# Optimization experiments

Hardware: AMD Instinct MI355X
Metric: run time of the kernel (lower is better)

Reference implementation:

```python
import jax, jax.numpy as jnp
import numpy as np

B, L, S = 8192, 1024, 3
OUTSIDE, TM_HELIX, INSIDE = 0, 1, 2


def setup_inputs() -> dict:
    key = jax.random.key(0)
    k1, k2 = jax.random.split(key)
    emissions = jax.random.normal(k1, (B, L, S), dtype=jnp.float32)
    tags = jax.random.randint(k2, (B, L), 0, S)
    mask = jnp.ones((B, L), dtype=jnp.float32)
    t = np.zeros((S, S), dtype=np.float32)
    t[OUTSIDE, INSIDE] = -5.0
    t[INSIDE, OUTSIDE] = -5.0
    t[OUTSIDE, TM_HELIX] = 1.0
    t[INSIDE, TM_HELIX] = 1.0
    t[TM_HELIX, OUTSIDE] = 1.0
    t[TM_HELIX, INSIDE] = 1.0
    transitions = jnp.asarray(t)
    return {"emissions": emissions, "mask": mask, "transitions": transitions, "tags": tags}


def _score_sentence(emissions, tags, mask, transitions):
    # emission score of the gold tag at every position: (B, L)
    em_score = jnp.take_along_axis(emissions, tags[..., None], axis=2)[..., 0]
    # transition score between consecutive gold tags: (B, L-1)
    trans_score = transitions[tags[:, :-1], tags[:, 1:]]
    return em_score[:, 0] * mask[:, 0] + jnp.sum(
        (trans_score + em_score[:, 1:]) * mask[:, 1:], axis=1
    )


def _forward_alg(emissions, mask, transitions):
    def step(alpha, xs):
        em_t, m_t = xs  # (B, S), (B,)
        # scores[b, i, j] = alpha[b, i] + T[i, j] + em_t[b, j]
        scores = alpha[:, :, None] + transitions[None, :, :] + em_t[:, None, :]
        new_alpha = jax.nn.logsumexp(scores, axis=1)
        alpha = jnp.where(m_t[:, None] > 0, new_alpha, alpha)
        return alpha, None

    alpha0 = emissions[:, 0, :]
    xs = (jnp.swapaxes(emissions[:, 1:, :], 0, 1),  # (L-1, B, S)
          jnp.swapaxes(mask[:, 1:], 0, 1))          # (L-1, B)
    alpha, _ = jax.lax.scan(step, alpha0, xs)
    return jax.nn.logsumexp(alpha, axis=1)  # (B,)


def reference(emissions, mask, transitions, tags):
    logZ = _forward_alg(emissions, mask, transitions)
    gold = _score_sentence(emissions, tags, mask, transitions)
    return jnp.mean(logZ - gold)
```

## Files before the change

### kernel.cpp

```cpp
#include <hip/hip_runtime.h>


#define LOG2E 1.4426950408889634f
#define LN2   0.6931471805599453f

constexpr int B = 8192;
constexpr int L = 1024;
constexpr int SEQS_PER_BLOCK = 4;

__device__ __forceinline__ float fexp2(float x) { return __builtin_amdgcn_exp2f(x); }
__device__ __forceinline__ float flog2(float x) { return __builtin_amdgcn_logf(x); }

__device__ __forceinline__ float mux3(float x0, float x1, float x2, int i) {
  return (i == 0) ? x0 : ((i == 1) ? x1 : x2);
}
__device__ __forceinline__ float trmux(const float* __restrict__ T2, int p, int c) {
  const float r0 = mux3(T2[0], T2[1], T2[2], c);
  const float r1 = mux3(T2[3], T2[4], T2[5], c);
  const float r2 = mux3(T2[6], T2[7], T2[8], c);
  return mux3(r0, r1, r2, p);
}

__device__ __forceinline__ void matmul3(float* __restrict__ D,
                                        const float* __restrict__ A,
                                        const float* __restrict__ Bm) {
  #pragma unroll
  for (int i = 0; i < 3; ++i)
    #pragma unroll
    for (int j = 0; j < 3; ++j)
      D[i * 3 + j] = A[i * 3 + 0] * Bm[0 * 3 + j] +
                     A[i * 3 + 1] * Bm[1 * 3 + j] +
                     A[i * 3 + 2] * Bm[2 * 3 + j];
}

__device__ __forceinline__ void renorm3(float* __restrict__ P, float& scale) {
  float m = P[0];
  #pragma unroll
  for (int e = 1; e < 9; ++e) m = fmaxf(m, P[e]);
  int ex;
  (void)frexpf(m, &ex);
  #pragma unroll
  for (int e = 0; e < 9; ++e) P[e] = ldexpf(P[e], -ex);
  scale += (float)ex;
}

__global__ __launch_bounds__(256, 4) void crf_main(
    const float* __restrict__ em, const float* __restrict__ mask,
    const float* __restrict__ trans, const int* __restrict__ tags,
    float* __restrict__ out) {
  const int lane = threadIdx.x & 63;
  const int wid = threadIdx.x >> 6;
  const int b = blockIdx.x * SEQS_PER_BLOCK + wid;

  float T2[9], tk[9];
  #pragma unroll
  for (int e = 0; e < 9; ++e) {
    T2[e] = trans[e] * LOG2E;
    tk[e] = fexp2(T2[e]);
  }

  const float4* em4 = (const float4*)(em + (size_t)b * (L * 3));
  const float4* mk4 = (const float4*)(mask + (size_t)b * L);
  const int4*   tg4 = (const int4*)(tags + (size_t)b * L);

  float P[9] = {1.f, 0.f, 0.f, 0.f, 1.f, 0.f, 0.f, 0.f, 1.f};
  float scale = 0.f, gold = 0.f;
  float a0 = 0.f, a1 = 0.f, a2 = 0.f;
  float e0_sel = 0.f, mk0 = 0.f;
  int tag0 = 0, prev = 0;

  #pragma unroll
  for (int g = 0; g < 4; ++g) {
    const float4 x0 = em4[lane * 12 + 3 * g + 0];
    const float4 x1 = em4[lane * 12 + 3 * g + 1];
    const float4 x2 = em4[lane * 12 + 3 * g + 2];
    const float4 mm = mk4[lane * 4 + g];
    const int4   tt = tg4[lane * 4 + g];
    const float ef[12] = {x0.x, x0.y, x0.z, x0.w, x1.x, x1.y, x1.z, x1.w,
                          x2.x, x2.y, x2.z, x2.w};
    const float mf[4] = {mm.x, mm.y, mm.z, mm.w};
    const int   tf[4] = {tt.x, tt.y, tt.z, tt.w};

    #pragma unroll
    for (int j = 0; j < 4; ++j) {
      const int s = 4 * g + j;
      const float ev0 = ef[3 * j + 0] * LOG2E;
      const float ev1 = ef[3 * j + 1] * LOG2E;
      const float ev2 = ef[3 * j + 2] * LOG2E;
      const float m = mf[j];
      const int cur = tf[j];

      const float e = mux3(ev0, ev1, ev2, cur);
      if (s == 0) {
        e0_sel = e; mk0 = m; tag0 = cur;
      } else {
        gold = fmaf(trmux(T2, prev, cur) + e, m, gold);
      }
      prev = cur;

      const float w0 = fexp2(ev0);
      const float w1 = fexp2(ev1);
      const float w2 = fexp2(ev2);
      if (s == 0) { a0 = w0; a1 = w1; a2 = w2; }
      const bool act = (m > 0.f) && !(s == 0 && lane == 0);
      const float M[9] = {tk[0] * w0, tk[1] * w1, tk[2] * w2,
                          tk[3] * w0, tk[4] * w1, tk[5] * w2,
                          tk[6] * w0, tk[7] * w1, tk[8] * w2};
      float N[9];
      matmul3(N, P, M);
      #pragma unroll
      for (int e2 = 0; e2 < 9; ++e2) P[e2] = act ? N[e2] : P[e2];

      if (s == 7 || s == 15) renorm3(P, scale);
    }
  }

  const int prevLast = __shfl_up(prev, 1);
  if (lane == 0) gold = fmaf(e0_sel, mk0, gold);
  else           gold = fmaf(trmux(T2, prevLast, tag0) + e0_sel, mk0, gold);
  #pragma unroll
  for (int d = 1; d < 64; d <<= 1) gold += __shfl_xor(gold, d, 64);

  #pragma unroll
  for (int d = 1; d < 64; d <<= 1) {
    float o[9];
    #pragma unroll
    for (int e = 0; e < 9; ++e) o[e] = __shfl_xor(P[e], d, 64);
    const float osc = __shfl_xor(scale, d, 64);
    const bool later = (lane & d) != 0;
    float A[9], Bm[9];
    #pragma unroll
    for (int e = 0; e < 9; ++e) {
      A[e]  = later ? o[e] : P[e];
      Bm[e] = later ? P[e] : o[e];
    }
    float N[9];
    matmul3(N, A, Bm);
    #pragma unroll
    for (int e = 0; e < 9; ++e) P[e] = N[e];
    scale += osc;
  }

  __shared__ float red[SEQS_PER_BLOCK];
  if (lane == 0) {
    const float z = a0 * (P[0] + P[1] + P[2]) +
                    a1 * (P[3] + P[4] + P[5]) +
                    a2 * (P[6] + P[7] + P[8]);
    red[wid] = LN2 * (scale + flog2(z) - gold);
  }
  __syncthreads();
  if (threadIdx.x == 0) {
    const float s = red[0] + red[1] + red[2] + red[3];
    atomicAdd(out, s * (1.0f / (float)B));
  }
}

extern "C" void kernel_launch(void* const* d_in, const int* in_sizes, int n_in,
                              void* d_out, int out_size, void* d_ws, size_t ws_size,
                              hipStream_t stream) {
  const float* em    = (const float*)d_in[0];
  const float* mask  = (const float*)d_in[1];
  const float* trans = (const float*)d_in[2];
  const int*   tags  = (const int*)d_in[3];
  float* out = (float*)d_out;

  hipMemsetAsync(out, 0, sizeof(float), stream);
  crf_main<<<B / SEQS_PER_BLOCK, 256, 0, stream>>>(em, mask, trans, tags, out);
}
```

Before: 197.2 us.

## Split sequences into chunks per lane with LDS staging and separate combine kernel

Replaces the one-wave-per-sequence scheme, which used a 64-lane shuffle scan of 3x3 matrices, with one lane per sequence handling a 128-position chunk. There are 8 chunks per sequence, and the chunk results go to a workspace. Emission, mask and tag loads are staged through LDS with a one-step register prefetch to keep global accesses coalesced. A second kernel composes the chunk matrices sequentially per sequence and reduces. The mask select becomes arithmetic blending inside the matrix step. In exchange the change adds a workspace round trip and a second launch, and only 512 blocks of 128 threads run in the main kernel, which may underfill the GPU.

```diff
diff --git a/kernel.cpp b/kernel.cpp
--- a/kernel.cpp
+++ b/kernel.cpp
@@ -5,154 +5,205 @@
 #define LN2   0.6931471805599453f
 
 constexpr int B = 8192;
-constexpr int L = 1024;
-constexpr int SEQS_PER_BLOCK = 4;
-
-__device__ __forceinline__ float fexp2(float x) { return __builtin_amdgcn_exp2f(x); }
-__device__ __forceinline__ float flog2(float x) { return __builtin_amdgcn_logf(x); }
-
-__device__ __forceinline__ float mux3(float x0, float x1, float x2, int i) {
-  return (i == 0) ? x0 : ((i == 1) ? x1 : x2);
-}
-__device__ __forceinline__ float trmux(const float* __restrict__ T2, int p, int c) {
-  const float r0 = mux3(T2[0], T2[1], T2[2], c);
-  const float r1 = mux3(T2[3], T2[4], T2[5], c);
-  const float r2 = mux3(T2[6], T2[7], T2[8], c);
-  return mux3(r0, r1, r2, p);
-}
-
-__device__ __forceinline__ void matmul3(float* __restrict__ D,
-                                        const float* __restrict__ A,
-                                        const float* __restrict__ Bm) {
-  #pragma unroll
-  for (int i = 0; i < 3; ++i)
-    #pragma unroll
-    for (int j = 0; j < 3; ++j)
-      D[i * 3 + j] = A[i * 3 + 0] * Bm[0 * 3 + j] +
-                     A[i * 3 + 1] * Bm[1 * 3 + j] +
-                     A[i * 3 + 2] * Bm[2 * 3 + j];
-}
-
-__device__ __forceinline__ void renorm3(float* __restrict__ P, float& scale) {
+constexpr int NCHUNK = 8;
+constexpr int NSUB = 32;
+constexpr int EM_ST = 14;
+constexpr int MK_ST = 6;
+constexpr int TG_ST = 6;
+constexpr int NF = 13;
+
+__device__ __forceinline__ float fexp2(float x){ return __builtin_amdgcn_exp2f(x); }
+__device__ __forceinline__ float flog2(float x){ return __builtin_amdgcn_logf(x); }
+__device__ __forceinline__ float mux3(float a,float b,float c,int i){
+  return i==0 ? a : (i==1 ? b : c);
+}
+__device__ __forceinline__ float trmux(const float* __restrict__ T2,int p,int c){
+  const float r0 = mux3(T2[0],T2[1],T2[2],c);
+  const float r1 = mux3(T2[3],T2[4],T2[5],c);
+  const float r2 = mux3(T2[6],T2[7],T2[8],c);
+  return mux3(r0,r1,r2,p);
+}
+
+__device__ __forceinline__ void stepP(float* __restrict__ P,
+                                      const float* __restrict__ tk,
+                                      float w0, float w1, float w2, float g){
+  const float c1 = 1.f - g;
+  const float u0 = w0*g, u1 = w1*g, u2 = w2*g;
+  float N0,N1,N2,N3,N4,N5,N6,N7,N8;
+  { const float m0=fmaf(tk[0],u0,c1), m1=tk[3]*u0, m2=tk[6]*u0;
+    N0 = P[0]*m0 + P[1]*m1 + P[2]*m2;
+    N3 = P[3]*m0 + P[4]*m1 + P[5]*m2;
+    N6 = P[6]*m0 + P[7]*m1 + P[8]*m2; }
+  { const float m0=tk[1]*u1, m1=fmaf(tk[4],u1,c1), m2=tk[7]*u1;
+    N1 = P[0]*m0 + P[1]*m1 + P[2]*m2;
+    N4 = P[3]*m0 + P[4]*m1 + P[5]*m2;
+    N7 = P[6]*m0 + P[7]*m1 + P[8]*m2; }
+  { const float m0=tk[2]*u2, m1=tk[5]*u2, m2=fmaf(tk[8],u2,c1);
+    N2 = P[0]*m0 + P[1]*m1 + P[2]*m2;
+    N5 = P[3]*m0 + P[4]*m1 + P[5]*m2;
+    N8 = P[6]*m0 + P[7]*m1 + P[8]*m2; }
+  P[0]=N0; P[1]=N1; P[2]=N2; P[3]=N3; P[4]=N4;
+  P[5]=N5; P[6]=N6; P[7]=N7; P[8]=N8;
+}
+
+__device__ __forceinline__ void renorm3(float* __restrict__ P, float& scale){
   float m = P[0];
   #pragma unroll
-  for (int e = 1; e < 9; ++e) m = fmaxf(m, P[e]);
+  for (int e=1;e<9;++e) m = fmaxf(m, P[e]);
   int ex;
   (void)frexpf(m, &ex);
   #pragma unroll
-  for (int e = 0; e < 9; ++e) P[e] = ldexpf(P[e], -ex);
+  for (int e=0;e<9;++e) P[e] = ldexpf(P[e], -ex);
   scale += (float)ex;
 }
 
-__global__ __launch_bounds__(256, 4) void crf_main(
+__global__ __launch_bounds__(128) void crf_chunk(
     const float* __restrict__ em, const float* __restrict__ mask,
     const float* __restrict__ trans, const int* __restrict__ tags,
+    float* __restrict__ ws) {
+  __shared__ float s_em[2][64*EM_ST];
+  __shared__ float s_mk[2][64*MK_ST];
+  __shared__ int   s_tg[2][64*TG_ST];
+
+  const int lane = threadIdx.x & 63;
+  const int wid  = threadIdx.x >> 6;
+  const int sg   = blockIdx.x & 63;
+  const int c    = blockIdx.x >> 6;
+  const int seqbase = sg*128 + wid*64;
+  const int seq = seqbase + lane;
+  const bool c0 = (c == 0);
+
+  float* emL = s_em[wid];
+  float* mkL = s_mk[wid];
+  int*   tgL = s_tg[wid];
+
+  float T2[9], tk[9];
+  #pragma unroll
+  for (int e=0;e<9;++e){ T2[e] = trans[e]*LOG2E; tk[e] = fexp2(T2[e]); }
+
+  const float4* em4 = (const float4*)em;
+  const float4* mk4 = (const float4*)mask;
+  const int4*   tg4 = (const int4*)tags;
+
+  int wa0, wa1, wa2; size_t gb0, gb1, gb2;
+  {
+    int K, r, col;
+    K = lane;        r = K/3; col = K-3*r; wa0 = r*EM_ST+col*4; gb0 = (size_t)(seqbase+r)*768 + (size_t)c*96 + col;
+    K = 64 + lane;   r = K/3; col = K-3*r; wa1 = r*EM_ST+col*4; gb1 = (size_t)(seqbase+r)*768 + (size_t)c*96 + col;
+    K = 128 + lane;  r = K/3; col = K-3*r; wa2 = r*EM_ST+col*4; gb2 = (size_t)(seqbase+r)*768 + (size_t)c*96 + col;
+  }
+  const size_t mb = (size_t)seq*256 + (size_t)c*32;
+
+  float4 sA = em4[gb0], sBv = em4[gb1], sC = em4[gb2];
+  float4 sM = mk4[mb];
+  int4   sT = tg4[mb];
+
+  float P[9] = {1.f,0.f,0.f, 0.f,1.f,0.f, 0.f,0.f,1.f};
+  float scale = 0.f, gold = 0.f;
+  float a0 = 0.f, a1 = 0.f, a2 = 0.f, m0s = 0.f;
+  int tag0 = 0, prev = 0;
+
+  for (int sub = 0; sub < NSUB; ++sub) {
+    { float2* w = (float2*)&emL[wa0]; w[0]=make_float2(sA.x,sA.y);  w[1]=make_float2(sA.z,sA.w); }
+    { float2* w = (float2*)&emL[wa1]; w[0]=make_float2(sBv.x,sBv.y);w[1]=make_float2(sBv.z,sBv.w); }
+    { float2* w = (float2*)&emL[wa2]; w[0]=make_float2(sC.x,sC.y);  w[1]=make_float2(sC.z,sC.w); }
+    { float2* w = (float2*)&mkL[lane*MK_ST]; w[0]=make_float2(sM.x,sM.y); w[1]=make_float2(sM.z,sM.w); }
+    { int2*   w = (int2*)&tgL[lane*TG_ST];   w[0]=make_int2(sT.x,sT.y);   w[1]=make_int2(sT.z,sT.w); }
+
+    if (sub + 1 < NSUB) {
+      const int o = (sub+1)*3;
+      sA = em4[gb0 + o]; sBv = em4[gb1 + o]; sC = em4[gb2 + o];
+      sM = mk4[mb + sub + 1];
+      sT = tg4[mb + sub + 1];
+    }
+
+    const float2* ep = (const float2*)&emL[lane*EM_ST];
+    const float2* mp = (const float2*)&mkL[lane*MK_ST];
+    const int2*   tp = (const int2*)&tgL[lane*TG_ST];
+    #pragma unroll
+    for (int p = 0; p < 2; ++p) {
+      const float2 ea = ep[3*p], eb = ep[3*p+1], ec = ep[3*p+2];
+      const float2 mm = mp[p];
+      const int2   tt = tp[p];
+      #pragma unroll
+      for (int jj = 0; jj < 2; ++jj) {
+        const float ev0 = (jj ? eb.y : ea.x) * LOG2E;
+        const float ev1 = (jj ? ec.x : ea.y) * LOG2E;
+        const float ev2 = (jj ? ec.y : eb.x) * LOG2E;
+        const float m   = jj ? mm.y : mm.x;
+        const int   cur = jj ? tt.y : tt.x;
+        const bool first = (sub == 0) && (p == 0) && (jj == 0);
+
+        const float e = mux3(ev0, ev1, ev2, cur);
+        if (first) { tag0 = cur; m0s = m; gold = e * m; }
+        else       gold = fmaf(trmux(T2, prev, cur) + e, m, gold);
+        prev = cur;
+
+        const float w0 = fexp2(ev0), w1 = fexp2(ev1), w2 = fexp2(ev2);
+        if (first && c0) { a0 = w0; a1 = w1; a2 = w2; }
+        const bool act = (m > 0.f) && !(first && c0);
+        stepP(P, tk, w0, w1, w2, act ? 1.f : 0.f);
+      }
+    }
+    if (sub & 1) renorm3(P, scale);
+  }
+
+  float* f = ws + (size_t)c*NF*8192 + seq;
+  f[0*8192]=P[0]; f[1*8192]=P[1]; f[2*8192]=P[2];
+  f[3*8192]=P[3]; f[4*8192]=P[4]; f[5*8192]=P[5];
+  f[6*8192]=P[6]; f[7*8192]=P[7]; f[8*8192]=P[8];
+  f[9*8192]=scale; f[10*8192]=gold; f[11*8192]=m0s;
+  f[12*8192]=(float)(tag0 + 4*prev);
+  if (c0) {
+    float* aw = ws + (size_t)NF*NCHUNK*8192;
+    aw[seq] = a0; aw[8192+seq] = a1; aw[2*8192+seq] = a2;
+  }
+}
+
+__global__ __launch_bounds__(256) void crf_combine(
+    const float* __restrict__ trans, const float* __restrict__ ws,
     float* __restrict__ out) {
-  const int lane = threadIdx.x & 63;
-  const int wid = threadIdx.x >> 6;
-  const int b = blockIdx.x * SEQS_PER_BLOCK + wid;
-
-  float T2[9], tk[9];
-  #pragma unroll
-  for (int e = 0; e < 9; ++e) {
-    T2[e] = trans[e] * LOG2E;
-    tk[e] = fexp2(T2[e]);
-  }
-
-  const float4* em4 = (const float4*)(em + (size_t)b * (L * 3));
-  const float4* mk4 = (const float4*)(mask + (size_t)b * L);
-  const int4*   tg4 = (const int4*)(tags + (size_t)b * L);
-
-  float P[9] = {1.f, 0.f, 0.f, 0.f, 1.f, 0.f, 0.f, 0.f, 1.f};
-  float scale = 0.f, gold = 0.f;
-  float a0 = 0.f, a1 = 0.f, a2 = 0.f;
-  float e0_sel = 0.f, mk0 = 0.f;
-  int tag0 = 0, prev = 0;
-
-  #pragma unroll
-  for (int g = 0; g < 4; ++g) {
-    const float4 x0 = em4[lane * 12 + 3 * g + 0];
-    const float4 x1 = em4[lane * 12 + 3 * g + 1];
-    const float4 x2 = em4[lane * 12 + 3 * g + 2];
-    const float4 mm = mk4[lane * 4 + g];
-    const int4   tt = tg4[lane * 4 + g];
-    const float ef[12] = {x0.x, x0.y, x0.z, x0.w, x1.x, x1.y, x1.z, x1.w,
-                          x2.x, x2.y, x2.z, x2.w};
-    const float mf[4] = {mm.x, mm.y, mm.z, mm.w};
-    const int   tf[4] = {tt.x, tt.y, tt.z, tt.w};
-
-    #pragma unroll
-    for (int j = 0; j < 4; ++j) {
-      const int s = 4 * g + j;
-      const float ev0 = ef[3 * j + 0] * LOG2E;
-      const float ev1 = ef[3 * j + 1] * LOG2E;
-      const float ev2 = ef[3 * j + 2] * LOG2E;
-      const float m = mf[j];
-      const int cur = tf[j];
-
-      const float e = mux3(ev0, ev1, ev2, cur);
-      if (s == 0) {
-        e0_sel = e; mk0 = m; tag0 = cur;
-      } else {
-        gold = fmaf(trmux(T2, prev, cur) + e, m, gold);
-      }
-      prev = cur;
-
-      const float w0 = fexp2(ev0);
-      const float w1 = fexp2(ev1);
-      const float w2 = fexp2(ev2);
-      if (s == 0) { a0 = w0; a1 = w1; a2 = w2; }
-      const bool act = (m > 0.f) && !(s == 0 && lane == 0);
-      const float M[9] = {tk[0] * w0, tk[1] * w1, tk[2] * w2,
-                          tk[3] * w0, tk[4] * w1, tk[5] * w2,
-                          tk[6] * w0, tk[7] * w1, tk[8] * w2};
-      float N[9];
-      matmul3(N, P, M);
-      #pragma unroll
-      for (int e2 = 0; e2 < 9; ++e2) P[e2] = act ? N[e2] : P[e2];
-
-      if (s == 7 || s == 15) renorm3(P, scale);
-    }
-  }
-
-  const int prevLast = __shfl_up(prev, 1);
-  if (lane == 0) gold = fmaf(e0_sel, mk0, gold);
-  else           gold = fmaf(trmux(T2, prevLast, tag0) + e0_sel, mk0, gold);
-  #pragma unroll
-  for (int d = 1; d < 64; d <<= 1) gold += __shfl_xor(gold, d, 64);
-
-  #pragma unroll
-  for (int d = 1; d < 64; d <<= 1) {
-    float o[9];
-    #pragma unroll
-    for (int e = 0; e < 9; ++e) o[e] = __shfl_xor(P[e], d, 64);
-    const float osc = __shfl_xor(scale, d, 64);
-    const bool later = (lane & d) != 0;
-    float A[9], Bm[9];
-    #pragma unroll
-    for (int e = 0; e < 9; ++e) {
-      A[e]  = later ? o[e] : P[e];
-      Bm[e] = later ? P[e] : o[e];
-    }
-    float N[9];
-    matmul3(N, A, Bm);
-    #pragma unroll
-    for (int e = 0; e < 9; ++e) P[e] = N[e];
-    scale += osc;
-  }
-
-  __shared__ float red[SEQS_PER_BLOCK];
-  if (lane == 0) {
-    const float z = a0 * (P[0] + P[1] + P[2]) +
-                    a1 * (P[3] + P[4] + P[5]) +
-                    a2 * (P[6] + P[7] + P[8]);
-    red[wid] = LN2 * (scale + flog2(z) - gold);
-  }
+  __shared__ float red[4];
+  const int seq = blockIdx.x*256 + threadIdx.x;
+
+  float T2[9];
+  #pragma unroll
+  for (int e=0;e<9;++e) T2[e] = trans[e]*LOG2E;
+
+  const float* aw = ws + (size_t)NF*NCHUNK*8192;
+  float al0 = aw[seq], al1 = aw[8192+seq], al2 = aw[2*8192+seq];
+  float sc = 0.f, gold = 0.f;
+  int lastTag = 0;
+
+  for (int c = 0; c < NCHUNK; ++c) {
+    const float* f = ws + (size_t)c*NF*8192 + seq;
+    const float p0=f[0*8192], p1=f[1*8192], p2=f[2*8192];
+    const float p3=f[3*8192], p4=f[4*8192], p5=f[5*8192];
+    const float p6=f[6*8192], p7=f[7*8192], p8=f[8*8192];
+    const float csc=f[9*8192], gp=f[10*8192], m0=f[11*8192];
+    const int tp = (int)f[12*8192];
+    const int t0 = tp & 3, tl = tp >> 2;
+
+    gold += gp + (c > 0 ? trmux(T2, lastTag, t0) * m0 : 0.f);
+    lastTag = tl;
+
+    const float n0 = al0*p0 + al1*p3 + al2*p6;
+    const float n1 = al0*p1 + al1*p4 + al2*p7;
+    const float n2 = al0*p2 + al1*p5 + al2*p8;
+    float mx = fmaxf(n0, fmaxf(n1, n2));
+    int ex; (void)frexpf(mx, &ex);
+    al0 = ldexpf(n0, -ex); al1 = ldexpf(n1, -ex); al2 = ldexpf(n2, -ex);
+    sc += csc + (float)ex;
+  }
+
+  const float z = al0 + al1 + al2;
+  float v = LN2 * (sc + flog2(z) - gold);
+  #pragma unroll
+  for (int d = 1; d < 64; d <<= 1) v += __shfl_xor(v, d, 64);
+  if ((threadIdx.x & 63) == 0) red[threadIdx.x >> 6] = v;
   __syncthreads();
-  if (threadIdx.x == 0) {
-    const float s = red[0] + red[1] + red[2] + red[3];
-    atomicAdd(out, s * (1.0f / (float)B));
-  }
+  if (threadIdx.x == 0)
+    atomicAdd(out, (red[0]+red[1]+red[2]+red[3]) * (1.0f/(float)B));
 }
 
 extern "C" void kernel_launch(void* const* d_in, const int* in_sizes, int n_in,
@@ -163,7 +214,9 @@
   const float* trans = (const float*)d_in[2];
   const int*   tags  = (const int*)d_in[3];
   float* out = (float*)d_out;
+  float* ws  = (float*)d_ws;
 
   hipMemsetAsync(out, 0, sizeof(float), stream);
-  crf_main<<<B / SEQS_PER_BLOCK, 256, 0, stream>>>(em, mask, trans, tags, out);
-}
+  crf_chunk<<<64*NCHUNK, 128, 0, stream>>>(em, mask, trans, tags, ws);
+  crf_combine<<<B/256, 256, 0, stream>>>(trans, ws, out);
+}
```

Result: slower. 228.8 us (+16.1%).
